# Performance work log

Hardware: AMD Instinct MI355X
Metric: run time of the kernel (lower is better)

The kernel has to match this reference:

```python
import jax, jax.numpy as jnp
import numpy as np

R0 = 1.0
DIM_A, DIM_V, DIM_D = 32, 32, 32
N_NODES = 20000
N_EDGES = 640000


def radial_encode_8(r, r0):
    # 8 Gaussian radial basis functions on the edge length |r_ij|
    d = jnp.linalg.norm(r, axis=-1)                      # [E]
    centers = jnp.linspace(0.0, r0, 8)                   # [8]
    width = r0 / 8.0
    return jnp.exp(-(((d[..., None] - centers) / width) ** 2))  # [E,8]


def tens_sigmoid_vec(v):
    # norm-saturating nonlinearity for rank-1 tensors (direction-preserving)
    n2 = jnp.sum(v * v, axis=-1, keepdims=True)
    return v * jax.lax.rsqrt(1.0 + n2)


def setup_inputs() -> dict:
    key = jax.random.key(0)
    ks = jax.random.split(key, 12)

    def lin(k, fan_in, fan_out):
        return jax.random.normal(k, (fan_in, fan_out), jnp.float32) / np.float32(np.sqrt(fan_in))

    return dict(
        r_ij=jax.random.normal(ks[0], (N_EDGES, 3), jnp.float32),
        w_rad=lin(ks[1], 8, DIM_A), b_rad=jnp.zeros((DIM_A,), jnp.float32),
        w_direct=lin(ks[2], DIM_A, DIM_A),
        w1=lin(ks[3], DIM_A, 2 * DIM_A), b1=jnp.zeros((2 * DIM_A,), jnp.float32),
        w2=lin(ks[4], 2 * DIM_A, 2 * DIM_A), b2=jnp.zeros((2 * DIM_A,), jnp.float32),
        w3=lin(ks[5], 2 * DIM_A, DIM_A), b3=jnp.zeros((DIM_A,), jnp.float32),
        w_v=lin(ks[6], DIM_A, DIM_V),
        w_d=lin(ks[7], DIM_A, DIM_D),
        edges_src=jax.random.randint(ks[8], (N_EDGES,), 0, N_NODES),
        n_nodes=N_NODES,
    )


def reference(r_ij, w_rad, b_rad, w_direct, w1, b1, w2, b2, w3, b3, w_v, w_d,
              edges_src, n_nodes):
    lrelu = lambda x: jnp.where(x > 0, x, 0.1 * x)
    # radial MLP: Linear(8, a) -> MLP (lin_direct + 3-layer leakyrelu net)
    h = radial_encode_8(r_ij, R0) @ w_rad + b_rad                      # [E,a]
    rad = h @ w_direct + (lrelu(lrelu(h @ w1 + b1) @ w2 + b2) @ w3 + b3)  # [E,a]
    rs = tens_sigmoid_vec(r_ij * (7.0 / R0))                            # [E,3]

    seg = lambda x: jax.ops.segment_sum(x, edges_src, num_segments=n_nodes)
    A_a = seg(rad)                                                      # [N,a]
    A_v = seg(rad[:, :, None] * rs[:, None, :])                         # [N,a,3]
    # phi_d_ij = rad ⊗ rs ⊗ rs per edge  -> [E,a,3,3], then scatter-sum
    A_d = seg(rad[:, :, None, None] * rs[:, None, None, :] * rs[:, None, :, None])  # [N,a,3,3]

    out_v = jnp.einsum('nac,av->nvc', A_v, w_v)                         # TensLinear rank 1
    out_d = jnp.einsum('naij,ad->ndij', A_d, w_d)                       # TensLinear rank 2
    return A_a, out_v, out_d
```

## Files before the change

kernel.cpp:

```cpp
#include <hip/hip_runtime.h>
#include <hip/hip_bf16.h>
#include <hip/hip_fp16.h>
#include <math.h>


#define TSIZE 8192
#define DMAX  2.0f
#define EPB   4
#define HB    128
#define TILE  10240
#define NPB   4
#define ROWB  512
#define ROWF  128

#define O_WRAD 0
#define O_BRAD 256
#define O_WDIR 288
#define O_W1   1312
#define O_B1   3360
#define O_W2   3424
#define O_B2   7520
#define O_W3   7584
#define O_B3   9632
#define O_WV   9664
#define O_WD   10688
#define W_TOT  11712

typedef float        f32x4 __attribute__((ext_vector_type(4)));
typedef unsigned int u32x2 __attribute__((ext_vector_type(2)));

struct TE { float r, v, d; };

__device__ __forceinline__ float lrelu(float x) { return x > 0.0f ? x : 0.1f * x; }

__device__ __forceinline__ float ldf(const void* p, int i, bool f32) {
    return f32 ? ((const float*)p)[i]
               : __uint_as_float(((unsigned int)((const unsigned short*)p)[i]) << 16);
}
__device__ __forceinline__ void stf(void* p, size_t i, float v, bool f32) {
    if (f32) ((float*)p)[i] = v;
    else     ((__hip_bfloat16*)p)[i] = __float2bfloat16(v);
}

__device__ __forceinline__ bool detect_f32(const void* r) {
    const unsigned short* p = (const unsigned short*)r;
    int bad = 0;
#pragma unroll 8
    for (int i = 0; i < 128; i++) {
        float v = __uint_as_float(((unsigned int)p[i]) << 16);
        bad |= (!isfinite(v) || fabsf(v) > 1e5f) ? 1 : 0;
    }
    return bad != 0;
}

__device__ __forceinline__ void load8x16(
    const void* p0, const void* p1, const void* p2, const void* p3,
    const void* p4, const void* p5, const void* p6, const void* p7,
    f32x4& q0, f32x4& q1, f32x4& q2, f32x4& q3,
    f32x4& q4, f32x4& q5, f32x4& q6, f32x4& q7) {
    asm volatile(
        "global_load_dwordx4 %0, %8, off\n\t"
        "global_load_dwordx4 %1, %9, off\n\t"
        "global_load_dwordx4 %2, %10, off\n\t"
        "global_load_dwordx4 %3, %11, off\n\t"
        "global_load_dwordx4 %4, %12, off\n\t"
        "global_load_dwordx4 %5, %13, off\n\t"
        "global_load_dwordx4 %6, %14, off\n\t"
        "global_load_dwordx4 %7, %15, off\n\t"
        "s_waitcnt vmcnt(0)"
        : "=&v"(q0), "=&v"(q1), "=&v"(q2), "=&v"(q3),
          "=&v"(q4), "=&v"(q5), "=&v"(q6), "=&v"(q7)
        : "v"(p0), "v"(p1), "v"(p2), "v"(p3),
          "v"(p4), "v"(p5), "v"(p6), "v"(p7));
}

__global__ void k_prep(const void* __restrict__ r_ij,
                       const void* w_rad, const void* b_rad, const void* w_direct,
                       const void* w1, const void* b1, const void* w2, const void* b2,
                       const void* w3, const void* b3, const void* w_v, const void* w_d,
                       float* __restrict__ wcat, int* __restrict__ flag,
                       int* __restrict__ counts, int N) {
    const int b = blockIdx.x;
    if (b == 0) {
        if (threadIdx.x == 0) flag[0] = detect_f32(r_ij) ? 1 : 0;
    } else if (b <= 11) {
        const bool f32 = detect_f32(r_ij);
        const void* src; int cnt; int off;
        switch (b) {
            case 1:  src = w_rad;    cnt = 256;  off = O_WRAD; break;
            case 2:  src = b_rad;    cnt = 32;   off = O_BRAD; break;
            case 3:  src = w_direct; cnt = 1024; off = O_WDIR; break;
            case 4:  src = w1;       cnt = 2048; off = O_W1;   break;
            case 5:  src = b1;       cnt = 64;   off = O_B1;   break;
            case 6:  src = w2;       cnt = 4096; off = O_W2;   break;
            case 7:  src = b2;       cnt = 64;   off = O_B2;   break;
            case 8:  src = w3;       cnt = 2048; off = O_W3;   break;
            case 9:  src = b3;       cnt = 32;   off = O_B3;   break;
            case 10: src = w_v;      cnt = 1024; off = O_WV;   break;
            default: src = w_d;      cnt = 1024; off = O_WD;   break;
        }
        for (int i = threadIdx.x; i < cnt; i += blockDim.x)
            wcat[off + i] = ldf(src, i, f32);
    } else if (counts) {
        int i = (b - 12) * blockDim.x + threadIdx.x;
        if (i < N) counts[i] = 0;
    }
}

__global__ void __launch_bounds__(64 * EPB) k_table(const float* __restrict__ wcat,
                                                    float* __restrict__ tabI) {
    __shared__ float Lh[EPB][32], Lt1[EPB][64], Lt2[EPB][64], Lrad[EPB][32];

    const int s = threadIdx.x >> 6;
    const int j = threadIdx.x & 63;
    const int e = blockIdx.x * EPB + s;
    const float d = (float)e * (DMAX / (float)(TSIZE - 1));

    float enc[8];
#pragma unroll
    for (int k = 0; k < 8; k++) {
        float t = (d - (float)k * (1.0f / 7.0f)) * 8.0f;
        enc[k] = expf(-t * t);
    }

    if (j < 32) {
        float hv = wcat[O_BRAD + j];
#pragma unroll
        for (int k = 0; k < 8; k++) hv = fmaf(enc[k], wcat[O_WRAD + k * 32 + j], hv);
        Lh[s][j] = hv;
    }
    __syncthreads();

    {
        float v = wcat[O_B1 + j];
#pragma unroll
        for (int i = 0; i < 32; i++) v = fmaf(Lh[s][i], wcat[O_W1 + i * 64 + j], v);
        Lt1[s][j] = lrelu(v);
    }
    __syncthreads();

    {
        float v = wcat[O_B2 + j];
#pragma unroll
        for (int i = 0; i < 64; i++) v = fmaf(Lt1[s][i], wcat[O_W2 + i * 64 + j], v);
        Lt2[s][j] = lrelu(v);
    }
    __syncthreads();

    if (j < 32) {
        float v = wcat[O_B3 + j];
#pragma unroll
        for (int i = 0; i < 64; i++) v = fmaf(Lt2[s][i], wcat[O_W3 + i * 32 + j], v);
#pragma unroll
        for (int i = 0; i < 32; i++) v = fmaf(Lh[s][i], wcat[O_WDIR + i * 32 + j], v);
        Lrad[s][j] = v;
    }
    __syncthreads();

    if (j < 32) {
        float sv = 0.0f, sd = 0.0f;
#pragma unroll
        for (int i = 0; i < 32; i++) {
            float ri = Lrad[s][i];
            sv = fmaf(ri, wcat[O_WV + i * 32 + j], sv);
            sd = fmaf(ri, wcat[O_WD + i * 32 + j], sd);
        }
        float* row = tabI + (size_t)e * ROWF + j * 4;
        row[0] = Lrad[s][j];
        row[1] = sv;
        row[2] = sd;
        row[3] = 0.0f;
    }
}

__global__ void __launch_bounds__(256) k_hist(const int* __restrict__ src, int E,
                                              int chunk,
                                              unsigned short* __restrict__ cnt,
                                              int N) {
    __shared__ int lcnt[TILE];
    const int b = blockIdx.x % HB;
    const int t = blockIdx.x / HB;
    const int lo = b * chunk;
    const int hi = min(lo + chunk, E);
    const int t0 = t * TILE;
    const int tl = min(TILE, N - t0);

    for (int i = threadIdx.x; i < tl; i += 256) lcnt[i] = 0;
    __syncthreads();
    for (int e = lo + threadIdx.x; e < hi; e += 256) {
        const int s = src[e] - t0;
        if ((unsigned)s < (unsigned)tl) atomicAdd(&lcnt[s], 1);
    }
    __syncthreads();
    unsigned short* out = cnt + (size_t)(t * HB + b) * TILE;
    for (int i = threadIdx.x; i < tl; i += 256)
        out[i] = (unsigned short)lcnt[i];
}

__global__ void __launch_bounds__(64) k_colscan(unsigned short* __restrict__ cnt,
                                                int* __restrict__ tot,
                                                int* __restrict__ coarse, int N) {
    const int lane = threadIdx.x;
    const int n = blockIdx.x * 64 + lane;
    int run = 0;
    if (n < N) {
        const int t = n / TILE;
        const int nl = n % TILE;
        unsigned short* col = cnt + (size_t)(t * HB) * TILE + nl;
#pragma unroll 4
        for (int b = 0; b < HB; b++) {
            int c = col[(size_t)b * TILE];
            col[(size_t)b * TILE] = (unsigned short)run;
            run += c;
        }
        tot[n] = run;
    }
    int s = run;
    for (int off = 32; off > 0; off >>= 1) s += __shfl_down(s, off);
    if (lane == 0) coarse[blockIdx.x] = s;
}

__global__ void __launch_bounds__(64) k_scan2(const int* __restrict__ tot,
                                              const int* __restrict__ coarse,
                                              int* __restrict__ rowstart, int N) {
    const int lane = threadIdx.x;
    const int b = blockIdx.x;
    int cp = 0;
    for (int j = lane; j < b; j += 64) cp += coarse[j];
    for (int off = 32; off > 0; off >>= 1) cp += __shfl_down(cp, off);
    const int cpre = __shfl(cp, 0);

    const int n = b * 64 + lane;
    const int v = (n < N) ? tot[n] : 0;
    int inc = v;
    for (int off = 1; off < 64; off <<= 1) {
        int y = __shfl_up(inc, off);
        if (lane >= off) inc += y;
    }
    if (n < N) rowstart[n] = cpre + inc - v;
    if (n == N - 1) rowstart[N] = cpre + inc;
}

template <bool P16>
__global__ void __launch_bounds__(256) k_place(
        const int* __restrict__ src, int E, int chunk,
        const unsigned short* __restrict__ cnt, const int* __restrict__ rowstart,
        const void* __restrict__ r_ij, const int* __restrict__ flag,
        void* __restrict__ epsv, int N) {
    __shared__ int cur[TILE];
    const int b = blockIdx.x % HB;
    const int t = blockIdx.x / HB;
    const int lo = b * chunk;
    const int hi = min(lo + chunk, E);
    const int t0 = t * TILE;
    const int tl = min(TILE, N - t0);
    const bool f32 = flag[0] != 0;

    const unsigned short* base = cnt + (size_t)(t * HB + b) * TILE;
    for (int i = threadIdx.x; i < tl; i += 256)
        cur[i] = rowstart[t0 + i] + (int)base[i];
    __syncthreads();
    for (int e = lo + threadIdx.x; e < hi; e += 256) {
        const int s = src[e] - t0;
        if ((unsigned)s < (unsigned)tl) {
            const int pos = atomicAdd(&cur[s], 1);
            const float x = ldf(r_ij, 3 * e + 0, f32);
            const float y = ldf(r_ij, 3 * e + 1, f32);
            const float z = ldf(r_ij, 3 * e + 2, f32);
            const float d2 = x * x + y * y + z * z;
            const float inv = rsqrtf(1.0f + 49.0f * d2);
            const float u = fminf(sqrtf(d2), DMAX) * ((float)(TSIZE - 1) / DMAX);
            const int ti = (int)(u + 0.5f);
            const float rs0 = 7.0f * x * inv, rs1 = 7.0f * y * inv,
                        rs2 = 7.0f * z * inv;
            if (P16) {
                ((float4*)epsv)[pos] =
                    make_float4(rs0, rs1, rs2, __int_as_float(ti * ROWB));
            } else {
                const unsigned int h0 = __half_as_ushort(__float2half(rs0));
                const unsigned int h1 = __half_as_ushort(__float2half(rs1));
                const unsigned int h2 = __half_as_ushort(__float2half(rs2));
                ((uint2*)epsv)[pos] =
                    make_uint2(h0 | (h1 << 16), h2 | ((unsigned)ti << 16));
            }
        }
    }
}

#define ACC16(Q, U)                                                           \
    do {                                                                      \
        const float x = (Q).x, y = (Q).y, z = (Q).z;                          \
        accA += (U).x;                                                        \
        v0 += (U).y * x; v1 += (U).y * y; v2 += (U).y * z;                    \
        const float _tx = (U).z * x, _ty = (U).z * y, _tz = (U).z * z;        \
        d00 += _tx * x; d01 += _tx * y; d02 += _tx * z;                       \
        d10 += _ty * x; d11 += _ty * y; d12 += _ty * z;                       \
        d20 += _tz * x; d21 += _tz * y; d22 += _tz * z;                       \
    } while (0)

template <bool P16>
__global__ void __launch_bounds__(64 * NPB, 4) k_nodes2(
    const void* __restrict__ epsv,
    const int* __restrict__ rowstart,
    const float* __restrict__ tabI,
    const int* __restrict__ flag,
    void* __restrict__ out, int N) {
    const int wave = threadIdx.x >> 6;
    const int lane = threadIdx.x & 63;
    const int n0 = (blockIdx.x * NPB + wave) * 2;
    const int a = lane & 31;
    const int half = lane >> 5;
    const int myn = n0 + half;
    const bool f32 = flag[0] != 0;
    const char* tabA = (const char*)tabI + a * 16;

    int s0 = 0, s1 = 0;
    if (myn < N) { s0 = rowstart[myn]; s1 = rowstart[myn + 1]; }
    const int mylen = s1 - s0;
    const int lenA = __shfl(mylen, 0);
    const int lenB = __shfl(mylen, 32);
    const int minl = min(lenA, lenB);
    const int maxl = max(lenA, lenB);
    const int mclamp = max(mylen - 1, 0);

    float accA = 0.f, v0 = 0.f, v1 = 0.f, v2 = 0.f;
    float d00 = 0.f, d01 = 0.f, d02 = 0.f,
          d10 = 0.f, d11 = 0.f, d12 = 0.f,
          d20 = 0.f, d21 = 0.f, d22 = 0.f;

    if (P16) {
        int i = 0;
        for (; i + 8 <= minl; i += 8) {
            const char* pb = (const char*)epsv + (size_t)(s0 + i) * 16;
            f32x4 q0, q1, q2, q3, q4, q5, q6, q7;
            load8x16(pb, pb + 16, pb + 32, pb + 48,
                     pb + 64, pb + 80, pb + 96, pb + 112,
                     q0, q1, q2, q3, q4, q5, q6, q7);
            f32x4 u0, u1, u2, u3, u4, u5, u6, u7;
            load8x16(tabA + __float_as_int(q0.w), tabA + __float_as_int(q1.w),
                     tabA + __float_as_int(q2.w), tabA + __float_as_int(q3.w),
                     tabA + __float_as_int(q4.w), tabA + __float_as_int(q5.w),
                     tabA + __float_as_int(q6.w), tabA + __float_as_int(q7.w),
                     u0, u1, u2, u3, u4, u5, u6, u7);
            ACC16(q0, u0); ACC16(q1, u1); ACC16(q2, u2); ACC16(q3, u3);
            ACC16(q4, u4); ACC16(q5, u5); ACC16(q6, u6); ACC16(q7, u7);
        }
        for (; i < maxl; i += 8) {
            float m0, m1, m2, m3, m4, m5, m6, m7;
#define TIDX(K) ((i + K) < mylen ? (i + K) : mclamp)
#define TPTR(K) ((const char*)epsv + (size_t)(s0 + TIDX(K)) * 16)
            m0 = (i + 0 < mylen) ? 1.f : 0.f;
            m1 = (i + 1 < mylen) ? 1.f : 0.f;
            m2 = (i + 2 < mylen) ? 1.f : 0.f;
            m3 = (i + 3 < mylen) ? 1.f : 0.f;
            m4 = (i + 4 < mylen) ? 1.f : 0.f;
            m5 = (i + 5 < mylen) ? 1.f : 0.f;
            m6 = (i + 6 < mylen) ? 1.f : 0.f;
            m7 = (i + 7 < mylen) ? 1.f : 0.f;
            f32x4 q0, q1, q2, q3, q4, q5, q6, q7;
            load8x16(TPTR(0), TPTR(1), TPTR(2), TPTR(3),
                     TPTR(4), TPTR(5), TPTR(6), TPTR(7),
                     q0, q1, q2, q3, q4, q5, q6, q7);
#undef TPTR
#undef TIDX
            f32x4 u0, u1, u2, u3, u4, u5, u6, u7;
            load8x16(tabA + __float_as_int(q0.w), tabA + __float_as_int(q1.w),
                     tabA + __float_as_int(q2.w), tabA + __float_as_int(q3.w),
                     tabA + __float_as_int(q4.w), tabA + __float_as_int(q5.w),
                     tabA + __float_as_int(q6.w), tabA + __float_as_int(q7.w),
                     u0, u1, u2, u3, u4, u5, u6, u7);
#define SAPX(K)                                                               \
            do { f32x4 uu = u##K; uu.x *= m##K; uu.y *= m##K; uu.z *= m##K;   \
                 ACC16(q##K, uu); } while (0)
            SAPX(0); SAPX(1); SAPX(2); SAPX(3);
            SAPX(4); SAPX(5); SAPX(6); SAPX(7);
#undef SAPX
        }
    } else {
        for (int i = 0; i < maxl; i++) {
            if (i < mylen) {
                const u32x2 qh = *((const u32x2*)epsv + (s0 + i));
                const float x = __half2float(__ushort_as_half(
                    (unsigned short)(qh.x & 0xffffu)));
                const float y = __half2float(__ushort_as_half(
                    (unsigned short)(qh.x >> 16)));
                const float z = __half2float(__ushort_as_half(
                    (unsigned short)(qh.y & 0xffffu)));
                const TE t = *(const TE*)(tabA + (int)(qh.y >> 16) * ROWB);
                accA += t.r;
                v0 += t.v * x; v1 += t.v * y; v2 += t.v * z;
                const float _tx = t.d * x, _ty = t.d * y, _tz = t.d * z;
                d00 += _tx * x; d01 += _tx * y; d02 += _tx * z;
                d10 += _ty * x; d11 += _ty * y; d12 += _ty * z;
                d20 += _tz * x; d21 += _tz * y; d22 += _tz * z;
            }
        }
    }

    if (myn >= N) return;
    const size_t baseV = (size_t)N * 32;
    const size_t baseD = (size_t)N * 128;
    stf(out, (size_t)myn * 32 + a, accA, f32);
    const size_t vb = baseV + (size_t)myn * 96 + a * 3;
    stf(out, vb + 0, v0, f32);
    stf(out, vb + 1, v1, f32);
    stf(out, vb + 2, v2, f32);
    const size_t db = baseD + (size_t)myn * 288 + a * 9;
    stf(out, db + 0, d00, f32);
    stf(out, db + 1, d01, f32);
    stf(out, db + 2, d02, f32);
    stf(out, db + 3, d10, f32);
    stf(out, db + 4, d11, f32);
    stf(out, db + 5, d12, f32);
    stf(out, db + 6, d20, f32);
    stf(out, db + 7, d21, f32);
    stf(out, db + 8, d22, f32);
}

__global__ void k_rank_g(const int* __restrict__ src, int* __restrict__ counts,
                         int* __restrict__ rank, int E) {
    int e = blockIdx.x * blockDim.x + threadIdx.x;
    if (e < E) rank[e] = atomicAdd(&counts[src[e]], 1);
}
__global__ void k_scan_g(const int* __restrict__ counts, int* __restrict__ rowstart,
                         int N, int E) {
    __shared__ int part[1024];
    const int t = threadIdx.x;
    const int CH = (N + 1023) / 1024;
    const int lo = t * CH;
    const int hi = min(lo + CH, N);
    int s = 0;
    for (int i = lo; i < hi; i++) s += counts[i];
    part[t] = s;
    __syncthreads();
    for (int off = 1; off < 1024; off <<= 1) {
        int v = part[t];
        int w = (t >= off) ? part[t - off] : 0;
        __syncthreads();
        part[t] = v + w;
        __syncthreads();
    }
    int run = (t == 0) ? 0 : part[t - 1];
    for (int i = lo; i < hi; i++) { rowstart[i] = run; run += counts[i]; }
    if (t == 0) rowstart[N] = E;
}
__global__ void k_place_g(const int* __restrict__ src, const int* __restrict__ rank,
                          const int* __restrict__ rowstart,
                          int* __restrict__ perm, int E) {
    int e = blockIdx.x * blockDim.x + threadIdx.x;
    if (e < E) perm[rowstart[src[e]] + rank[e]] = e;
}
__global__ void __launch_bounds__(256) k_nodes_fb(
    const int* __restrict__ perm, const void* __restrict__ r_ij,
    const int* __restrict__ rowstart, const float* __restrict__ tabI,
    const int* __restrict__ flag, void* __restrict__ out, int N) {
    const int wave = threadIdx.x >> 6;
    const int lane = threadIdx.x & 63;
    const int n = blockIdx.x * 4 + wave;
    if (n >= N) return;
    const int a = lane & 31;
    const bool hi = (lane >> 5) != 0;
    const bool f32 = flag[0] != 0;
    const int s0 = rowstart[n], s1 = rowstart[n + 1];
    float accR = 0.f, acc1 = 0.f, acc2 = 0.f, acc3 = 0.f,
          acc4 = 0.f, acc5 = 0.f, acc6 = 0.f;
    for (int idx = s0; idx < s1; idx++) {
        const int e = perm[idx];
        const float x0 = ldf(r_ij, 3 * e + 0, f32);
        const float y0 = ldf(r_ij, 3 * e + 1, f32);
        const float z0 = ldf(r_ij, 3 * e + 2, f32);
        const float d2 = x0 * x0 + y0 * y0 + z0 * z0;
        const float inv = rsqrtf(1.0f + 49.0f * d2);
        const float x = 7.0f * x0 * inv, y = 7.0f * y0 * inv, z = 7.0f * z0 * inv;
        const float u = fminf(sqrtf(d2), DMAX) * ((float)(TSIZE - 1) / DMAX);
        const int b = (int)(u + 0.5f) * ROWF + a * 4;
        const float ra = tabI[b], rv = tabI[b + 1], rd = tabI[b + 2];
        const float b1 = (hi ? rd : rv) * (hi ? y : 1.0f);
        const float b2 = rd * (hi ? z : x);
        accR += ra;
        acc1 += b1 * x; acc2 += b1 * y; acc3 += b1 * z;
        acc4 += b2 * x; acc5 += b2 * y; acc6 += b2 * z;
    }
    const size_t baseV = (size_t)N * 32;
    const size_t baseD = (size_t)N * 128;
    if (!hi) {
        stf(out, (size_t)n * 32 + a, accR, f32);
        const size_t vb = baseV + (size_t)n * 96 + a * 3;
        stf(out, vb + 0, acc1, f32);
        stf(out, vb + 1, acc2, f32);
        stf(out, vb + 2, acc3, f32);
        const size_t db = baseD + (size_t)n * 288 + a * 9;
        stf(out, db + 0, acc4, f32);
        stf(out, db + 1, acc5, f32);
        stf(out, db + 2, acc6, f32);
    } else {
        const size_t db = baseD + (size_t)n * 288 + a * 9;
        stf(out, db + 3, acc1, f32);
        stf(out, db + 4, acc2, f32);
        stf(out, db + 5, acc3, f32);
        stf(out, db + 6, acc4, f32);
        stf(out, db + 7, acc5, f32);
        stf(out, db + 8, acc6, f32);
    }
}

extern "C" void kernel_launch(void* const* d_in, const int* in_sizes, int n_in,
                              void* d_out, int out_size, void* d_ws, size_t ws_size,
                              hipStream_t stream) {
    const void* r_ij     = d_in[0];
    const void* w_rad    = d_in[1];
    const void* b_rad    = d_in[2];
    const void* w_direct = d_in[3];
    const void* w1       = d_in[4];
    const void* b1       = d_in[5];
    const void* w2       = d_in[6];
    const void* b2       = d_in[7];
    const void* w3       = d_in[8];
    const void* b3       = d_in[9];
    const void* w_v      = d_in[10];
    const void* w_d      = d_in[11];
    const int* edges_src = (const int*)d_in[12];

    const int E = in_sizes[12];
    const int N = out_size / 416;
    const int chunk = (E + HB - 1) / HB;
    const int ntiles = (N + TILE - 1) / TILE;
    const int NB = (N + 63) / 64;

    const size_t cntBytes  = (size_t)ntiles * HB * TILE * 2;
    const size_t tailBytes = ((size_t)W_TOT + 4) * 4 + (size_t)TSIZE * ROWF * 4
                           + cntBytes + ((size_t)N + NB + N + 1) * 4;
    const bool p16 = ws_size >= (size_t)E * 16 + tailBytes + 64;
    const bool p8  = !p16 && ws_size >= (size_t)E * 8 + tailBytes + 64;

    char* w = (char*)d_ws;
    if (p16 || p8) {
        const size_t slot = (size_t)E * (p16 ? 16 : 8);
        void* eps     = (void*)w;
        float* wcat   = (float*)(w + slot);
        int* flag     = (int*)(wcat + W_TOT);
        float* tabI   = (float*)(flag + 4);
        unsigned short* cnt = (unsigned short*)(tabI + (size_t)TSIZE * ROWF);
        int* tot      = (int*)((char*)cnt + cntBytes);
        int* coarse   = tot + N;
        int* rowstart = coarse + NB;

        const int nodeBlocks = (N + 2 * NPB - 1) / (2 * NPB);
        k_prep<<<12, 256, 0, stream>>>(
            r_ij, w_rad, b_rad, w_direct, w1, b1, w2, b2, w3, b3, w_v, w_d,
            wcat, flag, nullptr, N);
        k_table<<<TSIZE / EPB, 64 * EPB, 0, stream>>>(wcat, tabI);
        k_hist<<<HB * ntiles, 256, 0, stream>>>(edges_src, E, chunk, cnt, N);
        k_colscan<<<NB, 64, 0, stream>>>(cnt, tot, coarse, N);
        k_scan2<<<NB, 64, 0, stream>>>(tot, coarse, rowstart, N);
        if (p16) {
            k_place<true><<<HB * ntiles, 256, 0, stream>>>(
                edges_src, E, chunk, cnt, rowstart, r_ij, flag, eps, N);
            k_nodes2<true><<<nodeBlocks, 64 * NPB, 0, stream>>>(
                eps, rowstart, tabI, flag, d_out, N);
        } else {
            k_place<false><<<HB * ntiles, 256, 0, stream>>>(
                edges_src, E, chunk, cnt, rowstart, r_ij, flag, eps, N);
            k_nodes2<false><<<nodeBlocks, 64 * NPB, 0, stream>>>(
                eps, rowstart, tabI, flag, d_out, N);
        }
    } else {
        int* perm     = (int*)w;
        float* wcat   = (float*)(w + (size_t)E * 4);
        int* flag     = (int*)(wcat + W_TOT);
        float* tabI   = (float*)(flag + 4);
        int* counts   = (int*)(tabI + (size_t)TSIZE * ROWF);
        int* rowstart = counts + N;
        int* rank     = rowstart + N + 1;

        k_prep<<<12 + (N + 255) / 256, 256, 0, stream>>>(
            r_ij, w_rad, b_rad, w_direct, w1, b1, w2, b2, w3, b3, w_v, w_d,
            wcat, flag, counts, N);
        k_table<<<TSIZE / EPB, 64 * EPB, 0, stream>>>(wcat, tabI);
        k_rank_g<<<(E + 255) / 256, 256, 0, stream>>>(edges_src, counts, rank, E);
        k_scan_g<<<1, 1024, 0, stream>>>(counts, rowstart, N, E);
        k_place_g<<<(E + 255) / 256, 256, 0, stream>>>(edges_src, rank, rowstart,
                                                       perm, E);
        k_nodes_fb<<<(N + 3) / 4, 256, 0, stream>>>(
            perm, r_ij, rowstart, tabI, flag, d_out, N);
    }
}
```

Baseline: 201.0 us.

## Replace tiled histogram sort with global atomic rank sort and fuse prep into table

The tiled two-pass LDS histogram, column scan and two-level scan are replaced by a single global-atomic rank kernel, a single-block 1024-thread scan, and an edge-parallel placement kernel. The weight-gather prep kernel is folded into the table kernel, which now reads the raw weights directly and also zeroes the counts. The dtype flag buffer is dropped and each kernel detects the dtype itself. This cuts the launch count and the large count-matrix traffic, but it adds global atomic contention, a serial single-block scan, and a 16-bit rank that assumes no node has more than 65535 edges.

New measurement: 252.4 us. 1.26x slower.

```diff
diff --git a/kernel.cpp b/kernel.cpp
--- a/kernel.cpp
+++ b/kernel.cpp
@@ -7,24 +7,9 @@
 #define TSIZE 8192
 #define DMAX  2.0f
 #define EPB   4
-#define HB    128
-#define TILE  10240
 #define NPB   4
 #define ROWB  512
 #define ROWF  128
-
-#define O_WRAD 0
-#define O_BRAD 256
-#define O_WDIR 288
-#define O_W1   1312
-#define O_B1   3360
-#define O_W2   3424
-#define O_B2   7520
-#define O_W3   7584
-#define O_B3   9632
-#define O_WV   9664
-#define O_WD   10688
-#define W_TOT  11712
 
 typedef float        f32x4 __attribute__((ext_vector_type(4)));
 typedef unsigned int u32x2 __attribute__((ext_vector_type(2)));
@@ -74,43 +59,22 @@
           "v"(p4), "v"(p5), "v"(p6), "v"(p7));
 }
 
-__global__ void k_prep(const void* __restrict__ r_ij,
-                       const void* w_rad, const void* b_rad, const void* w_direct,
-                       const void* w1, const void* b1, const void* w2, const void* b2,
-                       const void* w3, const void* b3, const void* w_v, const void* w_d,
-                       float* __restrict__ wcat, int* __restrict__ flag,
-                       int* __restrict__ counts, int N) {
-    const int b = blockIdx.x;
-    if (b == 0) {
-        if (threadIdx.x == 0) flag[0] = detect_f32(r_ij) ? 1 : 0;
-    } else if (b <= 11) {
-        const bool f32 = detect_f32(r_ij);
-        const void* src; int cnt; int off;
-        switch (b) {
-            case 1:  src = w_rad;    cnt = 256;  off = O_WRAD; break;
-            case 2:  src = b_rad;    cnt = 32;   off = O_BRAD; break;
-            case 3:  src = w_direct; cnt = 1024; off = O_WDIR; break;
-            case 4:  src = w1;       cnt = 2048; off = O_W1;   break;
-            case 5:  src = b1;       cnt = 64;   off = O_B1;   break;
-            case 6:  src = w2;       cnt = 4096; off = O_W2;   break;
-            case 7:  src = b2;       cnt = 64;   off = O_B2;   break;
-            case 8:  src = w3;       cnt = 2048; off = O_W3;   break;
-            case 9:  src = b3;       cnt = 32;   off = O_B3;   break;
-            case 10: src = w_v;      cnt = 1024; off = O_WV;   break;
-            default: src = w_d;      cnt = 1024; off = O_WD;   break;
-        }
-        for (int i = threadIdx.x; i < cnt; i += blockDim.x)
-            wcat[off + i] = ldf(src, i, f32);
-    } else if (counts) {
-        int i = (b - 12) * blockDim.x + threadIdx.x;
+__global__ void __launch_bounds__(64 * EPB) k_table(
+    const void* __restrict__ r_ij,
+    const void* w_rad, const void* b_rad, const void* w_direct,
+    const void* w1, const void* b1, const void* w2, const void* b2,
+    const void* w3, const void* b3, const void* w_v, const void* w_d,
+    float* __restrict__ tabI, int* __restrict__ counts, int N) {
+    __shared__ float Lh[EPB][32], Lt1[EPB][64], Lt2[EPB][64], Lrad[EPB][32];
+
+    const int TB = TSIZE / EPB;
+    if (blockIdx.x >= TB) {
+        const int i = (blockIdx.x - TB) * (64 * EPB) + threadIdx.x;
         if (i < N) counts[i] = 0;
-    }
-}
-
-__global__ void __launch_bounds__(64 * EPB) k_table(const float* __restrict__ wcat,
-                                                    float* __restrict__ tabI) {
-    __shared__ float Lh[EPB][32], Lt1[EPB][64], Lt2[EPB][64], Lrad[EPB][32];
-
+        return;
+    }
+
+    const bool f32 = detect_f32(r_ij);
     const int s = threadIdx.x >> 6;
     const int j = threadIdx.x & 63;
     const int e = blockIdx.x * EPB + s;
@@ -124,35 +88,40 @@
     }
 
     if (j < 32) {
-        float hv = wcat[O_BRAD + j];
-#pragma unroll
-        for (int k = 0; k < 8; k++) hv = fmaf(enc[k], wcat[O_WRAD + k * 32 + j], hv);
+        float hv = ldf(b_rad, j, f32);
+#pragma unroll
+        for (int k = 0; k < 8; k++)
+            hv = fmaf(enc[k], ldf(w_rad, k * 32 + j, f32), hv);
         Lh[s][j] = hv;
     }
     __syncthreads();
 
     {
-        float v = wcat[O_B1 + j];
-#pragma unroll
-        for (int i = 0; i < 32; i++) v = fmaf(Lh[s][i], wcat[O_W1 + i * 64 + j], v);
+        float v = ldf(b1, j, f32);
+#pragma unroll
+        for (int i = 0; i < 32; i++)
+            v = fmaf(Lh[s][i], ldf(w1, i * 64 + j, f32), v);
         Lt1[s][j] = lrelu(v);
     }
     __syncthreads();
 
     {
-        float v = wcat[O_B2 + j];
-#pragma unroll
-        for (int i = 0; i < 64; i++) v = fmaf(Lt1[s][i], wcat[O_W2 + i * 64 + j], v);
+        float v = ldf(b2, j, f32);
+#pragma unroll
+        for (int i = 0; i < 64; i++)
+            v = fmaf(Lt1[s][i], ldf(w2, i * 64 + j, f32), v);
         Lt2[s][j] = lrelu(v);
     }
     __syncthreads();
 
     if (j < 32) {
-        float v = wcat[O_B3 + j];
-#pragma unroll
-        for (int i = 0; i < 64; i++) v = fmaf(Lt2[s][i], wcat[O_W3 + i * 32 + j], v);
-#pragma unroll
-        for (int i = 0; i < 32; i++) v = fmaf(Lh[s][i], wcat[O_WDIR + i * 32 + j], v);
+        float v = ldf(b3, j, f32);
+#pragma unroll
+        for (int i = 0; i < 64; i++)
+            v = fmaf(Lt2[s][i], ldf(w3, i * 32 + j, f32), v);
+#pragma unroll
+        for (int i = 0; i < 32; i++)
+            v = fmaf(Lh[s][i], ldf(w_direct, i * 32 + j, f32), v);
         Lrad[s][j] = v;
     }
     __syncthreads();
@@ -162,8 +131,8 @@
 #pragma unroll
         for (int i = 0; i < 32; i++) {
             float ri = Lrad[s][i];
-            sv = fmaf(ri, wcat[O_WV + i * 32 + j], sv);
-            sd = fmaf(ri, wcat[O_WD + i * 32 + j], sd);
+            sv = fmaf(ri, ldf(w_v, i * 32 + j, f32), sv);
+            sd = fmaf(ri, ldf(w_d, i * 32 + j, f32), sd);
         }
         float* row = tabI + (size_t)e * ROWF + j * 4;
         row[0] = Lrad[s][j];
@@ -173,117 +142,64 @@
     }
 }
 
-__global__ void __launch_bounds__(256) k_hist(const int* __restrict__ src, int E,
-                                              int chunk,
-                                              unsigned short* __restrict__ cnt,
-                                              int N) {
-    __shared__ int lcnt[TILE];
-    const int b = blockIdx.x % HB;
-    const int t = blockIdx.x / HB;
-    const int lo = b * chunk;
-    const int hi = min(lo + chunk, E);
-    const int t0 = t * TILE;
-    const int tl = min(TILE, N - t0);
-
-    for (int i = threadIdx.x; i < tl; i += 256) lcnt[i] = 0;
+__global__ void __launch_bounds__(256) k_rank(const int* __restrict__ src,
+                                              int* __restrict__ counts,
+                                              unsigned short* __restrict__ rank,
+                                              int E) {
+    const int e = blockIdx.x * 256 + threadIdx.x;
+    if (e < E) rank[e] = (unsigned short)atomicAdd(&counts[src[e]], 1);
+}
+
+__global__ void __launch_bounds__(1024) k_scan(const int* __restrict__ counts,
+                                               int* __restrict__ rowstart,
+                                               int N, int E) {
+    __shared__ int part[1024];
+    const int t = threadIdx.x;
+    const int CH = (N + 1023) / 1024;
+    const int lo = t * CH;
+    const int hi = min(lo + CH, N);
+    int s = 0;
+    for (int i = lo; i < hi; i++) s += counts[i];
+    part[t] = s;
     __syncthreads();
-    for (int e = lo + threadIdx.x; e < hi; e += 256) {
-        const int s = src[e] - t0;
-        if ((unsigned)s < (unsigned)tl) atomicAdd(&lcnt[s], 1);
-    }
-    __syncthreads();
-    unsigned short* out = cnt + (size_t)(t * HB + b) * TILE;
-    for (int i = threadIdx.x; i < tl; i += 256)
-        out[i] = (unsigned short)lcnt[i];
-}
-
-__global__ void __launch_bounds__(64) k_colscan(unsigned short* __restrict__ cnt,
-                                                int* __restrict__ tot,
-                                                int* __restrict__ coarse, int N) {
-    const int lane = threadIdx.x;
-    const int n = blockIdx.x * 64 + lane;
-    int run = 0;
-    if (n < N) {
-        const int t = n / TILE;
-        const int nl = n % TILE;
-        unsigned short* col = cnt + (size_t)(t * HB) * TILE + nl;
-#pragma unroll 4
-        for (int b = 0; b < HB; b++) {
-            int c = col[(size_t)b * TILE];
-            col[(size_t)b * TILE] = (unsigned short)run;
-            run += c;
-        }
-        tot[n] = run;
-    }
-    int s = run;
-    for (int off = 32; off > 0; off >>= 1) s += __shfl_down(s, off);
-    if (lane == 0) coarse[blockIdx.x] = s;
-}
-
-__global__ void __launch_bounds__(64) k_scan2(const int* __restrict__ tot,
-                                              const int* __restrict__ coarse,
-                                              int* __restrict__ rowstart, int N) {
-    const int lane = threadIdx.x;
-    const int b = blockIdx.x;
-    int cp = 0;
-    for (int j = lane; j < b; j += 64) cp += coarse[j];
-    for (int off = 32; off > 0; off >>= 1) cp += __shfl_down(cp, off);
-    const int cpre = __shfl(cp, 0);
-
-    const int n = b * 64 + lane;
-    const int v = (n < N) ? tot[n] : 0;
-    int inc = v;
-    for (int off = 1; off < 64; off <<= 1) {
-        int y = __shfl_up(inc, off);
-        if (lane >= off) inc += y;
-    }
-    if (n < N) rowstart[n] = cpre + inc - v;
-    if (n == N - 1) rowstart[N] = cpre + inc;
+    for (int off = 1; off < 1024; off <<= 1) {
+        int v = part[t];
+        int w = (t >= off) ? part[t - off] : 0;
+        __syncthreads();
+        part[t] = v + w;
+        __syncthreads();
+    }
+    int run = (t == 0) ? 0 : part[t - 1];
+    for (int i = lo; i < hi; i++) { rowstart[i] = run; run += counts[i]; }
+    if (t == 0) rowstart[N] = E;
 }
 
 template <bool P16>
-__global__ void __launch_bounds__(256) k_place(
-        const int* __restrict__ src, int E, int chunk,
-        const unsigned short* __restrict__ cnt, const int* __restrict__ rowstart,
-        const void* __restrict__ r_ij, const int* __restrict__ flag,
-        void* __restrict__ epsv, int N) {
-    __shared__ int cur[TILE];
-    const int b = blockIdx.x % HB;
-    const int t = blockIdx.x / HB;
-    const int lo = b * chunk;
-    const int hi = min(lo + chunk, E);
-    const int t0 = t * TILE;
-    const int tl = min(TILE, N - t0);
-    const bool f32 = flag[0] != 0;
-
-    const unsigned short* base = cnt + (size_t)(t * HB + b) * TILE;
-    for (int i = threadIdx.x; i < tl; i += 256)
-        cur[i] = rowstart[t0 + i] + (int)base[i];
-    __syncthreads();
-    for (int e = lo + threadIdx.x; e < hi; e += 256) {
-        const int s = src[e] - t0;
-        if ((unsigned)s < (unsigned)tl) {
-            const int pos = atomicAdd(&cur[s], 1);
-            const float x = ldf(r_ij, 3 * e + 0, f32);
-            const float y = ldf(r_ij, 3 * e + 1, f32);
-            const float z = ldf(r_ij, 3 * e + 2, f32);
-            const float d2 = x * x + y * y + z * z;
-            const float inv = rsqrtf(1.0f + 49.0f * d2);
-            const float u = fminf(sqrtf(d2), DMAX) * ((float)(TSIZE - 1) / DMAX);
-            const int ti = (int)(u + 0.5f);
-            const float rs0 = 7.0f * x * inv, rs1 = 7.0f * y * inv,
-                        rs2 = 7.0f * z * inv;
-            if (P16) {
-                ((float4*)epsv)[pos] =
-                    make_float4(rs0, rs1, rs2, __int_as_float(ti * ROWB));
-            } else {
-                const unsigned int h0 = __half_as_ushort(__float2half(rs0));
-                const unsigned int h1 = __half_as_ushort(__float2half(rs1));
-                const unsigned int h2 = __half_as_ushort(__float2half(rs2));
-                ((uint2*)epsv)[pos] =
-                    make_uint2(h0 | (h1 << 16), h2 | ((unsigned)ti << 16));
-            }
-        }
+__global__ void __launch_bounds__(256) k_place2(
+        const int* __restrict__ src, const unsigned short* __restrict__ rank,
+        const int* __restrict__ rowstart, const void* __restrict__ r_ij,
+        void* __restrict__ epsv, int E) {
+    const bool f32 = detect_f32(r_ij);
+    const int e = blockIdx.x * 256 + threadIdx.x;
+    if (e >= E) return;
+    const int pos = rowstart[src[e]] + (int)rank[e];
+    const float x = ldf(r_ij, 3 * e + 0, f32);
+    const float y = ldf(r_ij, 3 * e + 1, f32);
+    const float z = ldf(r_ij, 3 * e + 2, f32);
+    const float d2 = x * x + y * y + z * z;
+    const float inv = rsqrtf(1.0f + 49.0f * d2);
+    const float u = fminf(sqrtf(d2), DMAX) * ((float)(TSIZE - 1) / DMAX);
+    const int ti = (int)(u + 0.5f);
+    const float rs0 = 7.0f * x * inv, rs1 = 7.0f * y * inv, rs2 = 7.0f * z * inv;
+    if (P16) {
+        ((float4*)epsv)[pos] =
+            make_float4(rs0, rs1, rs2, __int_as_float(ti * ROWB));
+    } else {
+        const unsigned int h0 = __half_as_ushort(__float2half(rs0));
+        const unsigned int h1 = __half_as_ushort(__float2half(rs1));
+        const unsigned int h2 = __half_as_ushort(__float2half(rs2));
+        ((uint2*)epsv)[pos] =
+            make_uint2(h0 | (h1 << 16), h2 | ((unsigned)ti << 16));
     }
 }
 
@@ -303,7 +219,7 @@
     const void* __restrict__ epsv,
     const int* __restrict__ rowstart,
     const float* __restrict__ tabI,
-    const int* __restrict__ flag,
+    const void* __restrict__ r_ij,
     void* __restrict__ out, int N) {
     const int wave = threadIdx.x >> 6;
     const int lane = threadIdx.x & 63;
@@ -311,7 +227,7 @@
     const int a = lane & 31;
     const int half = lane >> 5;
     const int myn = n0 + half;
-    const bool f32 = flag[0] != 0;
+    const bool f32 = detect_f32(r_ij);
     const char* tabA = (const char*)tabI + a * 16;
 
     int s0 = 0, s1 = 0;
@@ -417,50 +333,23 @@
     stf(out, db + 8, d22, f32);
 }
 
-__global__ void k_rank_g(const int* __restrict__ src, int* __restrict__ counts,
-                         int* __restrict__ rank, int E) {
-    int e = blockIdx.x * blockDim.x + threadIdx.x;
-    if (e < E) rank[e] = atomicAdd(&counts[src[e]], 1);
-}
-__global__ void k_scan_g(const int* __restrict__ counts, int* __restrict__ rowstart,
-                         int N, int E) {
-    __shared__ int part[1024];
-    const int t = threadIdx.x;
-    const int CH = (N + 1023) / 1024;
-    const int lo = t * CH;
-    const int hi = min(lo + CH, N);
-    int s = 0;
-    for (int i = lo; i < hi; i++) s += counts[i];
-    part[t] = s;
-    __syncthreads();
-    for (int off = 1; off < 1024; off <<= 1) {
-        int v = part[t];
-        int w = (t >= off) ? part[t - off] : 0;
-        __syncthreads();
-        part[t] = v + w;
-        __syncthreads();
-    }
-    int run = (t == 0) ? 0 : part[t - 1];
-    for (int i = lo; i < hi; i++) { rowstart[i] = run; run += counts[i]; }
-    if (t == 0) rowstart[N] = E;
-}
-__global__ void k_place_g(const int* __restrict__ src, const int* __restrict__ rank,
-                          const int* __restrict__ rowstart,
-                          int* __restrict__ perm, int E) {
-    int e = blockIdx.x * blockDim.x + threadIdx.x;
-    if (e < E) perm[rowstart[src[e]] + rank[e]] = e;
+__global__ void __launch_bounds__(256) k_place_g(
+        const int* __restrict__ src, const unsigned short* __restrict__ rank,
+        const int* __restrict__ rowstart, int* __restrict__ perm, int E) {
+    const int e = blockIdx.x * 256 + threadIdx.x;
+    if (e < E) perm[rowstart[src[e]] + (int)rank[e]] = e;
 }
 __global__ void __launch_bounds__(256) k_nodes_fb(
     const int* __restrict__ perm, const void* __restrict__ r_ij,
     const int* __restrict__ rowstart, const float* __restrict__ tabI,
-    const int* __restrict__ flag, void* __restrict__ out, int N) {
+    void* __restrict__ out, int N) {
     const int wave = threadIdx.x >> 6;
     const int lane = threadIdx.x & 63;
     const int n = blockIdx.x * 4 + wave;
     if (n >= N) return;
     const int a = lane & 31;
     const bool hi = (lane >> 5) != 0;
-    const bool f32 = flag[0] != 0;
+    const bool f32 = detect_f32(r_ij);
     const int s0 = rowstart[n], s1 = rowstart[n + 1];
     float accR = 0.f, acc1 = 0.f, acc2 = 0.f, acc3 = 0.f,
           acc4 = 0.f, acc5 = 0.f, acc6 = 0.f;
@@ -523,65 +412,55 @@
 
     const int E = in_sizes[12];
     const int N = out_size / 416;
-    const int chunk = (E + HB - 1) / HB;
-    const int ntiles = (N + TILE - 1) / TILE;
-    const int NB = (N + 63) / 64;
-
-    const size_t cntBytes  = (size_t)ntiles * HB * TILE * 2;
-    const size_t tailBytes = ((size_t)W_TOT + 4) * 4 + (size_t)TSIZE * ROWF * 4
-                           + cntBytes + ((size_t)N + NB + N + 1) * 4;
-    const bool p16 = ws_size >= (size_t)E * 16 + tailBytes + 64;
-    const bool p8  = !p16 && ws_size >= (size_t)E * 8 + tailBytes + 64;
+    const int TB = TSIZE / EPB;
+    const int ZB = (N + 64 * EPB - 1) / (64 * EPB);
+    const int EB = (E + 255) / 256;
+    const int nodeBlocks = (N + 2 * NPB - 1) / (2 * NPB);
+
+    const size_t tailBytes = (size_t)TSIZE * ROWF * 4
+                           + ((size_t)N + N + 1) * 4 + (size_t)E * 2 + 64;
+    const bool p16 = ws_size >= (size_t)E * 16 + tailBytes;
+    const bool p8  = !p16 && ws_size >= (size_t)E * 8 + tailBytes;
 
     char* w = (char*)d_ws;
     if (p16 || p8) {
         const size_t slot = (size_t)E * (p16 ? 16 : 8);
-        void* eps     = (void*)w;
-        float* wcat   = (float*)(w + slot);
-        int* flag     = (int*)(wcat + W_TOT);
-        float* tabI   = (float*)(flag + 4);
-        unsigned short* cnt = (unsigned short*)(tabI + (size_t)TSIZE * ROWF);
-        int* tot      = (int*)((char*)cnt + cntBytes);
-        int* coarse   = tot + N;
-        int* rowstart = coarse + NB;
-
-        const int nodeBlocks = (N + 2 * NPB - 1) / (2 * NPB);
-        k_prep<<<12, 256, 0, stream>>>(
+        void* eps      = (void*)w;
+        float* tabI    = (float*)(w + slot);
+        int* counts    = (int*)(tabI + (size_t)TSIZE * ROWF);
+        int* rowstart  = counts + N;
+        unsigned short* rank = (unsigned short*)(rowstart + N + 1);
+
+        k_table<<<TB + ZB, 64 * EPB, 0, stream>>>(
             r_ij, w_rad, b_rad, w_direct, w1, b1, w2, b2, w3, b3, w_v, w_d,
-            wcat, flag, nullptr, N);
-        k_table<<<TSIZE / EPB, 64 * EPB, 0, stream>>>(wcat, tabI);
-        k_hist<<<HB * ntiles, 256, 0, stream>>>(edges_src, E, chunk, cnt, N);
-        k_colscan<<<NB, 64, 0, stream>>>(cnt, tot, coarse, N);
-        k_scan2<<<NB, 64, 0, stream>>>(tot, coarse, rowstart, N);
+            tabI, counts, N);
+        k_rank<<<EB, 256, 0, stream>>>(edges_src, counts, rank, E);
+        k_scan<<<1, 1024, 0, stream>>>(counts, rowstart, N, E);
         if (p16) {
-            k_place<true><<<HB * ntiles, 256, 0, stream>>>(
-                edges_src, E, chunk, cnt, rowstart, r_ij, flag, eps, N);
+            k_place2<true><<<EB, 256, 0, stream>>>(
+                edges_src, rank, rowstart, r_ij, eps, E);
             k_nodes2<true><<<nodeBlocks, 64 * NPB, 0, stream>>>(
-                eps, rowstart, tabI, flag, d_out, N);
+                eps, rowstart, tabI, r_ij, d_out, N);
         } else {
-            k_place<false><<<HB * ntiles, 256, 0, stream>>>(
-                edges_src, E, chunk, cnt, rowstart, r_ij, flag, eps, N);
+            k_place2<false><<<EB, 256, 0, stream>>>(
+                edges_src, rank, rowstart, r_ij, eps, E);
             k_nodes2<false><<<nodeBlocks, 64 * NPB, 0, stream>>>(
-                eps, rowstart, tabI, flag, d_out, N);
+                eps, rowstart, tabI, r_ij, d_out, N);
         }
     } else {
-        int* perm     = (int*)w;
-        float* wcat   = (float*)(w + (size_t)E * 4);
-        int* flag     = (int*)(wcat + W_TOT);
-        float* tabI   = (float*)(flag + 4);
-        int* counts   = (int*)(tabI + (size_t)TSIZE * ROWF);
-        int* rowstart = counts + N;
-        int* rank     = rowstart + N + 1;
-
-        k_prep<<<12 + (N + 255) / 256, 256, 0, stream>>>(
+        int* perm      = (int*)w;
+        float* tabI    = (float*)(w + (size_t)E * 4);
+        int* counts    = (int*)(tabI + (size_t)TSIZE * ROWF);
+        int* rowstart  = counts + N;
+        unsigned short* rank = (unsigned short*)(rowstart + N + 1);
+
+        k_table<<<TB + ZB, 64 * EPB, 0, stream>>>(
             r_ij, w_rad, b_rad, w_direct, w1, b1, w2, b2, w3, b3, w_v, w_d,
-            wcat, flag, counts, N);
-        k_table<<<TSIZE / EPB, 64 * EPB, 0, stream>>>(wcat, tabI);
-        k_rank_g<<<(E + 255) / 256, 256, 0, stream>>>(edges_src, counts, rank, E);
-        k_scan_g<<<1, 1024, 0, stream>>>(counts, rowstart, N, E);
-        k_place_g<<<(E + 255) / 256, 256, 0, stream>>>(edges_src, rank, rowstart,
-                                                       perm, E);
+            tabI, counts, N);
+        k_rank<<<EB, 256, 0, stream>>>(edges_src, counts, rank, E);
+        k_scan<<<1, 1024, 0, stream>>>(counts, rowstart, N, E);
+        k_place_g<<<EB, 256, 0, stream>>>(edges_src, rank, rowstart, perm, E);
         k_nodes_fb<<<(N + 3) / 4, 256, 0, stream>>>(
-            perm, r_ij, rowstart, tabI, flag, d_out, N);
-    }
-}
+            perm, r_ij, rowstart, tabI, d_out, N);
+    }
+}
```

## Software-pipeline edge payload and table gathers in node accumulation loop

Applied to the files above, without the earlier changes.

Splits the combined load-and-wait asm into load-only and explicit vmcnt wait helpers, then restructures the main per-node loop as a double-buffered pipeline. The next block of edge payloads is prefetched while the table gathers for the current block are in flight, so the dependent two-level load latency is overlapped. The extra live buffers raise register pressure, so launch bounds are relaxed from 4 to 3 blocks per CU, which may reduce occupancy.

Result: no change. 203.2 us (+1.1%).

```diff
diff --git a/kernel.cpp b/kernel.cpp
--- a/kernel.cpp
+++ b/kernel.cpp
@@ -72,6 +72,41 @@
           "=&v"(q4), "=&v"(q5), "=&v"(q6), "=&v"(q7)
         : "v"(p0), "v"(p1), "v"(p2), "v"(p3),
           "v"(p4), "v"(p5), "v"(p6), "v"(p7));
+}
+
+__device__ __forceinline__ void load8x16_nw(
+    const void* p0, const void* p1, const void* p2, const void* p3,
+    const void* p4, const void* p5, const void* p6, const void* p7,
+    f32x4& q0, f32x4& q1, f32x4& q2, f32x4& q3,
+    f32x4& q4, f32x4& q5, f32x4& q6, f32x4& q7) {
+    asm volatile(
+        "global_load_dwordx4 %0, %8, off\n\t"
+        "global_load_dwordx4 %1, %9, off\n\t"
+        "global_load_dwordx4 %2, %10, off\n\t"
+        "global_load_dwordx4 %3, %11, off\n\t"
+        "global_load_dwordx4 %4, %12, off\n\t"
+        "global_load_dwordx4 %5, %13, off\n\t"
+        "global_load_dwordx4 %6, %14, off\n\t"
+        "global_load_dwordx4 %7, %15, off"
+        : "=&v"(q0), "=&v"(q1), "=&v"(q2), "=&v"(q3),
+          "=&v"(q4), "=&v"(q5), "=&v"(q6), "=&v"(q7)
+        : "v"(p0), "v"(p1), "v"(p2), "v"(p3),
+          "v"(p4), "v"(p5), "v"(p6), "v"(p7));
+}
+
+__device__ __forceinline__ void waitv8(
+    f32x4& r0, f32x4& r1, f32x4& r2, f32x4& r3,
+    f32x4& r4, f32x4& r5, f32x4& r6, f32x4& r7) {
+    asm volatile("s_waitcnt vmcnt(8)"
+        : "+v"(r0), "+v"(r1), "+v"(r2), "+v"(r3),
+          "+v"(r4), "+v"(r5), "+v"(r6), "+v"(r7));
+}
+__device__ __forceinline__ void waitv0(
+    f32x4& r0, f32x4& r1, f32x4& r2, f32x4& r3,
+    f32x4& r4, f32x4& r5, f32x4& r6, f32x4& r7) {
+    asm volatile("s_waitcnt vmcnt(0)"
+        : "+v"(r0), "+v"(r1), "+v"(r2), "+v"(r3),
+          "+v"(r4), "+v"(r5), "+v"(r6), "+v"(r7));
 }
 
 __global__ void k_prep(const void* __restrict__ r_ij,
@@ -298,8 +333,29 @@
         d20 += _tz * x; d21 += _tz * y; d22 += _tz * z;                       \
     } while (0)
 
+#define P8ARGS(R) R##0, R##1, R##2, R##3, R##4, R##5, R##6, R##7
+#define LOADP_NW(R, IDX)                                                      \
+    do { const char* _pp = (const char*)epsv + (size_t)(IDX) * 16;            \
+         load8x16_nw(_pp, _pp + 16, _pp + 32, _pp + 48,                       \
+                     _pp + 64, _pp + 80, _pp + 96, _pp + 112, P8ARGS(R));     \
+    } while (0)
+#define LOADT_NW(R, Q)                                                        \
+    load8x16_nw(tabA + __float_as_int((Q##0).w),                              \
+                tabA + __float_as_int((Q##1).w),                              \
+                tabA + __float_as_int((Q##2).w),                              \
+                tabA + __float_as_int((Q##3).w),                              \
+                tabA + __float_as_int((Q##4).w),                              \
+                tabA + __float_as_int((Q##5).w),                              \
+                tabA + __float_as_int((Q##6).w),                              \
+                tabA + __float_as_int((Q##7).w),                              \
+                P8ARGS(R))
+#define ACCB(Q, T)                                                            \
+    do { ACC16(Q##0, T##0); ACC16(Q##1, T##1); ACC16(Q##2, T##2);             \
+         ACC16(Q##3, T##3); ACC16(Q##4, T##4); ACC16(Q##5, T##5);             \
+         ACC16(Q##6, T##6); ACC16(Q##7, T##7); } while (0)
+
 template <bool P16>
-__global__ void __launch_bounds__(64 * NPB, 4) k_nodes2(
+__global__ void __launch_bounds__(64 * NPB, 3) k_nodes2(
     const void* __restrict__ epsv,
     const int* __restrict__ rowstart,
     const float* __restrict__ tabI,
@@ -330,20 +386,40 @@
 
     if (P16) {
         int i = 0;
-        for (; i + 8 <= minl; i += 8) {
-            const char* pb = (const char*)epsv + (size_t)(s0 + i) * 16;
-            f32x4 q0, q1, q2, q3, q4, q5, q6, q7;
-            load8x16(pb, pb + 16, pb + 32, pb + 48,
-                     pb + 64, pb + 80, pb + 96, pb + 112,
-                     q0, q1, q2, q3, q4, q5, q6, q7);
-            f32x4 u0, u1, u2, u3, u4, u5, u6, u7;
-            load8x16(tabA + __float_as_int(q0.w), tabA + __float_as_int(q1.w),
-                     tabA + __float_as_int(q2.w), tabA + __float_as_int(q3.w),
-                     tabA + __float_as_int(q4.w), tabA + __float_as_int(q5.w),
-                     tabA + __float_as_int(q6.w), tabA + __float_as_int(q7.w),
-                     u0, u1, u2, u3, u4, u5, u6, u7);
-            ACC16(q0, u0); ACC16(q1, u1); ACC16(q2, u2); ACC16(q3, u3);
-            ACC16(q4, u4); ACC16(q5, u5); ACC16(q6, u6); ACC16(q7, u7);
+        if (minl >= 8) {
+            f32x4 pa0, pa1, pa2, pa3, pa4, pa5, pa6, pa7;
+            f32x4 pb0, pb1, pb2, pb3, pb4, pb5, pb6, pb7;
+            f32x4 tt0, tt1, tt2, tt3, tt4, tt5, tt6, tt7;
+            LOADP_NW(pa, s0);
+            waitv0(P8ARGS(pa));
+            for (; i + 24 <= minl; i += 16) {
+                LOADT_NW(tt, pa);
+                LOADP_NW(pb, s0 + i + 8);
+                waitv8(P8ARGS(tt));
+                ACCB(pa, tt);
+                waitv0(P8ARGS(pb));
+                LOADT_NW(tt, pb);
+                LOADP_NW(pa, s0 + i + 16);
+                waitv8(P8ARGS(tt));
+                ACCB(pb, tt);
+                waitv0(P8ARGS(pa));
+            }
+            if (i + 16 <= minl) {
+                LOADT_NW(tt, pa);
+                LOADP_NW(pb, s0 + i + 8);
+                waitv8(P8ARGS(tt));
+                ACCB(pa, tt);
+                waitv0(P8ARGS(pb));
+                LOADT_NW(tt, pb);
+                waitv0(P8ARGS(tt));
+                ACCB(pb, tt);
+                i += 16;
+            } else {
+                LOADT_NW(tt, pa);
+                waitv0(P8ARGS(tt));
+                ACCB(pa, tt);
+                i += 8;
+            }
         }
         for (; i < maxl; i += 8) {
             float m0, m1, m2, m3, m4, m5, m6, m7;
```
